# Optimization experiments

Measured on AMD Instinct MI355X. Metric: run time of the kernel, lower is better.

## Reference

```python
import jax, jax.numpy as jnp
import numpy as np

H = 1024          # rnn hidden dim
D = H // 2        # coarse/fine half
E = H // 8        # embed dim = 128
COND = H // 2     # conditioning (upsampled mel) dim = 512
EPS = 1e-5
TILE = 16


def _bn(x, scale, offset):
    # haiku BatchNorm, training mode: batch stats over (N, L)
    mean = jnp.mean(x, axis=(0, 1), keepdims=True)
    var = jnp.mean(jnp.square(x), axis=(0, 1), keepdims=True) - jnp.square(mean)
    return scale * (x - mean) * jax.lax.rsqrt(var + EPS) + offset


def _conv(x, w, rate=1):
    return jax.lax.conv_general_dilated(
        x, w, window_strides=(1,), padding='VALID', rhs_dilation=(rate,),
        dimension_numbers=('NWC', 'WIO', 'NWC'))


def _up(x, w, stride):
    # Conv1DTranspose with kernel 1, SAME padding: scatter x@w to positions i*stride
    N, L, _ = x.shape
    y = jnp.einsum('nlc,cd->nld', x, w)
    out = jnp.zeros((N, L, stride, y.shape[-1]), y.dtype).at[:, :, 0, :].set(y)
    return out.reshape(N, L * stride, y.shape[-1])


def _iw_mask():
    m = jnp.ones((COND + 3 * E, 3 * H), jnp.float32)
    for j in (0, 2, 4):  # coarse_t embed cannot see coarse half of u, r, e gates
        m = m.at[-E:, j * D:(j + 1) * D].set(0.0)
    return m


def _forward(x, mel, conv_in_w, bn0_s, bn0_o, dconv1_w, bn1_s, bn1_o,
             dconv2_w, bn2_s, bn2_o, up1_w, bn3_s, bn3_o, up2_w, bn4_s, bn4_o,
             up3_w, bn5_s, bn5_o, I_W, I_b, R_w, R_b,
             O1_w, O1_b, O2_w, O2_b, O3_w, O3_b, O4_w, O4_b, c_embed, f_embed):
    # ---- UpsampleNetwork ----
    h = jax.nn.relu(_bn(_conv(mel, conv_in_w), bn0_s, bn0_o))
    r1 = jax.nn.relu(_bn(_conv(h, dconv1_w, rate=2), bn1_s, bn1_o))
    h = h[:, 1:-1] + r1
    r2 = jax.nn.relu(_bn(_conv(h, dconv2_w, rate=4), bn2_s, bn2_o))
    h = h[:, 2:-2] + r2
    h = jax.nn.relu(_bn(_up(h, up1_w, 2), bn3_s, bn3_o))
    h = jax.nn.relu(_bn(_up(h, up2_w, 2), bn4_s, bn4_o))
    h = jax.nn.relu(_bn(_up(h, up3_w, 4), bn5_s, bn5_o))
    N, Lm, Dm = h.shape
    mel_up = jnp.tile(h[:, :, None, :], (1, 1, TILE, 1)).reshape(N, Lm * TILE, Dm)

    # ---- WaveRNNOriginal.__call__ (teacher-forced GRU) ----
    coarse, fine, coarse_t = x[..., 0], x[..., 1], x[..., 2]
    inputs = jnp.concatenate(
        (mel_up, c_embed[coarse], f_embed[fine], c_embed[coarse_t]), axis=-1)
    # precompute input projection for all timesteps  [N, L, 3H]
    ix = jnp.einsum('nli,ij->nlj', inputs, I_W * _iw_mask()) + I_b.reshape(1, 1, -1)
    ix_t = jnp.swapaxes(ix, 0, 1)  # time-major [L, N, 3H]
    h0 = jnp.zeros((N, H), ix.dtype)

    def step(hx, xt):
        u1, r1_, e1 = jnp.split(hx @ R_w + R_b, 3, axis=-1)
        u2, r2_, e2 = jnp.split(xt, 3, axis=-1)
        ut = jax.nn.sigmoid(u1 + u2)
        rt = jax.nn.sigmoid(r1_ + r2_)
        et = jnp.tanh(rt * e1 + e2)
        ht = ut * hx + (1.0 - ut) * et
        return ht, ht

    _, hs = jax.lax.scan(step, h0, ix_t)
    hs = jnp.swapaxes(hs, 0, 1)              # [N, L, H]
    yc, yf = jnp.split(hs, 2, axis=-1)       # [N, L, H/2] each
    clog = jax.nn.relu(yc @ O1_w + O1_b) @ O2_w + O2_b
    flog = jax.nn.relu(yf @ O3_w + O3_b) @ O4_w + O4_b
    logits = jnp.stack((clog, flog), axis=-1)  # [N, L, 256, 2]
    return jax.nn.log_softmax(logits, axis=-2)


def setup_inputs():
    key = jax.random.key(0)
    ks = jax.random.split(key, 24)
    n = jax.random.normal
    N, T = 2, 24
    L = (T - 8) * 256  # 4096
    inp = {
        'x': jax.random.randint(ks[0], (N, L, 3), 0, 256),
        'mel': n(ks[1], (N, T, 80), jnp.float32),
        'conv_in_w': n(ks[2], (3, 80, 512)) * 0.05,
        'dconv1_w': n(ks[3], (2, 512, 512)) * 0.05,
        'dconv2_w': n(ks[4], (2, 512, 512)) * 0.05,
        'up1_w': n(ks[5], (512, 512)) * 0.05,
        'up2_w': n(ks[6], (512, 512)) * 0.05,
        'up3_w': n(ks[7], (512, COND)) * 0.05,
        'I_W': n(ks[8], (COND + 3 * E, 3 * H)) * 0.03,
        'I_b': jnp.zeros((3 * H,)),
        'R_w': n(ks[9], (H, 3 * H)) * 0.03,
        'R_b': jnp.zeros((3 * H,)),
        'O1_w': n(ks[10], (D, D)) * 0.05,
        'O1_b': jnp.zeros((D,)),
        'O2_w': n(ks[11], (D, 256)) * 0.05,
        'O2_b': jnp.zeros((256,)),
        'O3_w': n(ks[12], (D, D)) * 0.05,
        'O3_b': jnp.zeros((D,)),
        'O4_w': n(ks[13], (D, 256)) * 0.05,
        'O4_b': jnp.zeros((256,)),
        'c_embed': n(ks[14], (256, E)) * 0.1,
        'f_embed': n(ks[15], (256, E)) * 0.1,
    }
    for i in range(6):
        c = COND if i == 5 else 512
        inp[f'bn{i}_s'] = jnp.ones((c,))
        inp[f'bn{i}_o'] = jnp.zeros((c,))
    return inp


def reference(x, mel, conv_in_w, dconv1_w, dconv2_w, up1_w, up2_w, up3_w,
              I_W, I_b, R_w, R_b, O1_w, O1_b, O2_w, O2_b, O3_w, O3_b,
              O4_w, O4_b, c_embed, f_embed,
              bn0_s, bn0_o, bn1_s, bn1_o, bn2_s, bn2_o,
              bn3_s, bn3_o, bn4_s, bn4_o, bn5_s, bn5_o):
    return _forward(x, mel, conv_in_w, bn0_s, bn0_o, dconv1_w, bn1_s, bn1_o,
                    dconv2_w, bn2_s, bn2_o, up1_w, bn3_s, bn3_o, up2_w, bn4_s,
                    bn4_o, up3_w, bn5_s, bn5_o, I_W, I_b, R_w, R_b,
                    O1_w, O1_b, O2_w, O2_b, O3_w, O3_b, O4_w, O4_b,
                    c_embed, f_embed)
```

## Files before the change

### kernel.cpp

```cpp
#include <hip/hip_runtime.h>
#include <hip/hip_bf16.h>
#include <math.h>

__device__ __forceinline__ float bf2f(unsigned short u) {
  unsigned int x = ((unsigned int)u) << 16;
  return __builtin_bit_cast(float, x);
}
__device__ __forceinline__ unsigned short f2bf(float f) {
  unsigned int x = __builtin_bit_cast(unsigned int, f);
  unsigned int lsb = (x >> 16) & 1u;
  x += 0x7fffu + lsb;
  return (unsigned short)(x >> 16);
}
template <bool BF>
__device__ __forceinline__ float ld(const void* p, size_t i) {
  if (BF) return bf2f(((const unsigned short*)p)[i]);
  return ((const float*)p)[i];
}

#define SCOPE_AGENT __HIP_MEMORY_SCOPE_AGENT
typedef unsigned long long ull;

__global__ void k_init(const unsigned int* bn0s, ull* sbuf, int* dt) {
  int t = threadIdx.x;
  for (int i = t; i < 4096; i += 256) sbuf[i] = 0ULL;
  if (t == 0) dt[0] = (bn0s[0] == 0x3F803F80u) ? 1 : 0;
}
__global__ void k_zero(uint4* hq4) {
  hq4[(size_t)blockIdx.x * 256 + threadIdx.x] = make_uint4(0u, 0u, 0u, 0u);
}

template <bool BF>
__device__ void conv_in_body(const void* mel, const void* w, float* out) {
  int idx = blockIdx.x * 256 + threadIdx.x;
  if (idx >= 2 * 22 * 512) return;
  int c = idx & 511, l = (idx >> 9) % 22, n = idx / (22 * 512);
  float acc = 0.f;
  for (int kw = 0; kw < 3; kw++) {
    size_t mrow = (size_t)(n * 24 + l + kw) * 80;
    size_t wrow = (size_t)kw * 80 * 512 + c;
#pragma unroll 4
    for (int i = 0; i < 80; i++)
      acc += ld<BF>(mel, mrow + i) * ld<BF>(w, wrow + (size_t)i * 512);
  }
  out[idx] = acc;
}
__global__ void k_conv_in(const void* mel, const void* w, float* out, const int* dt) {
  if (dt[0]) conv_in_body<true>(mel, w, out); else conv_in_body<false>(mel, w, out);
}

template <bool BF>
__device__ void dconv_body(const float* in, const void* w, float* out,
                           int Lin, int Lout, int rate) {
  int idx = blockIdx.x * 256 + threadIdx.x;
  if (idx >= 2 * Lout * 512) return;
  int c = idx & 511, l = (idx >> 9) % Lout, n = idx / (Lout * 512);
  float acc = 0.f;
  for (int kw = 0; kw < 2; kw++) {
    const float* irow = in + (n * Lin + l + kw * rate) * 512;
    size_t wrow = (size_t)kw * 512 * 512 + c;
#pragma unroll 4
    for (int i = 0; i < 512; i++)
      acc += irow[i] * ld<BF>(w, wrow + (size_t)i * 512);
  }
  out[idx] = acc;
}
__global__ void k_dconv(const float* in, const void* w, float* out,
                        int Lin, int Lout, int rate, const int* dt) {
  if (dt[0]) dconv_body<true>(in, w, out, Lin, Lout, rate);
  else dconv_body<false>(in, w, out, Lin, Lout, rate);
}

template <bool BF>
__device__ void up_body(const float* in, const void* w, float* out, int Lin, int stride) {
  int Lout = Lin * stride;
  int idx = blockIdx.x * 256 + threadIdx.x;
  if (idx >= 2 * Lout * 512) return;
  int c = idx & 511, lo = (idx >> 9) % Lout, n = idx / (Lout * 512);
  if (lo % stride) { out[idx] = 0.f; return; }
  const float* irow = in + (n * Lin + lo / stride) * 512;
  float acc = 0.f;
#pragma unroll 4
  for (int i = 0; i < 512; i++) acc += irow[i] * ld<BF>(w, (size_t)i * 512 + c);
  out[idx] = acc;
}
__global__ void k_up(const float* in, const void* w, float* out,
                     int Lin, int stride, const int* dt) {
  if (dt[0]) up_body<true>(in, w, out, Lin, stride);
  else up_body<false>(in, w, out, Lin, stride);
}

__global__ void k_bnstats(const float* __restrict__ x, float* __restrict__ st, int NL) {
  int c = blockIdx.x * 256 + threadIdx.x;
  if (c >= 512) return;
  float s = 0.f, s2 = 0.f;
  for (int r = 0; r < NL; r++) { float v = x[r * 512 + c]; s += v; s2 += v * v; }
  float m = s / (float)NL;
  float var = s2 / (float)NL - m * m;
  st[c] = m;
  st[512 + c] = rsqrtf(var + 1e-5f);
}

template <bool BF>
__device__ void bnrelu_body(const float* x, float* y, const float* st,
                            const void* sc, const void* of,
                            const float* res, int resL, int shift, int L) {
  int idx = blockIdx.x * 256 + threadIdx.x;
  if (idx >= 2 * L * 512) return;
  int c = idx & 511, l = (idx >> 9) % L, n = idx / (L * 512);
  float v = (x[idx] - st[c]) * st[512 + c] * ld<BF>(sc, c) + ld<BF>(of, c);
  v = fmaxf(v, 0.f);
  if (res) v += res[(n * resL + l + shift) * 512 + c];
  y[idx] = v;
}
__global__ void k_bnrelu(const float* x, float* y, const float* st,
                         const void* sc, const void* of,
                         const float* res, int resL, int shift, int L, const int* dt) {
  if (dt[0]) bnrelu_body<true>(x, y, st, sc, of, res, resL, shift, L);
  else bnrelu_body<false>(x, y, st, sc, of, res, resL, shift, L);
}

template <bool BF>
__device__ void M_body(const float* h5, const void* IW, const void* Ib,
                       const void* Rb, float* M, float* hl) {
  int bid = blockIdx.x;
  int rt = bid / 12, ct = bid % 12;
  int r0 = rt * 8, j = ct * 256 + threadIdx.x;
  const float4* src = (const float4*)(h5 + (size_t)r0 * 512);
  float4* dst = (float4*)hl;
  for (int q = threadIdx.x; q < 1024; q += 256) dst[q] = src[q];
  __syncthreads();
  float acc[8];
#pragma unroll
  for (int r = 0; r < 8; r++) acc[r] = 0.f;
  for (int k = 0; k < 512; k += 4) {
    float w0 = ld<BF>(IW, (size_t)k * 3072 + j);
    float w1 = ld<BF>(IW, (size_t)(k + 1) * 3072 + j);
    float w2 = ld<BF>(IW, (size_t)(k + 2) * 3072 + j);
    float w3 = ld<BF>(IW, (size_t)(k + 3) * 3072 + j);
#pragma unroll
    for (int r = 0; r < 8; r++) {
      float4 h4 = *(const float4*)(hl + r * 512 + k);
      acc[r] += h4.x * w0 + h4.y * w1 + h4.z * w2 + h4.w * w3;
    }
  }
  float bias = ld<BF>(Ib, j) + ((j < 2048) ? ld<BF>(Rb, j) : 0.f);
#pragma unroll
  for (int r = 0; r < 8; r++) M[(size_t)(r0 + r) * 3072 + j] = acc[r] + bias;
}
__global__ __launch_bounds__(256) void k_M(const float* h5, const void* IW,
                                           const void* Ib, const void* Rb,
                                           float* M, const int* dt) {
  __shared__ float hl[8 * 512];
  if (dt[0]) M_body<true>(h5, IW, Ib, Rb, M, hl);
  else M_body<false>(h5, IW, Ib, Rb, M, hl);
}

template <bool BF>
__device__ void T_body(const void* emb, const void* IW, int row0, int maskcoarse,
                       float* T, float* el) {
  int bid = blockIdx.x;
  int vt = bid / 12, ct = bid % 12;
  int v0 = vt * 8, j = ct * 256 + threadIdx.x;
  for (int q = threadIdx.x; q < 1024; q += 256)
    el[q] = ld<BF>(emb, (size_t)v0 * 128 + q);
  __syncthreads();
  float acc[8];
#pragma unroll
  for (int r = 0; r < 8; r++) acc[r] = 0.f;
  for (int k = 0; k < 128; k += 4) {
    float w0 = ld<BF>(IW, (size_t)(row0 + k) * 3072 + j);
    float w1 = ld<BF>(IW, (size_t)(row0 + k + 1) * 3072 + j);
    float w2 = ld<BF>(IW, (size_t)(row0 + k + 2) * 3072 + j);
    float w3 = ld<BF>(IW, (size_t)(row0 + k + 3) * 3072 + j);
#pragma unroll
    for (int r = 0; r < 8; r++) {
      float4 e4 = *(const float4*)(el + r * 128 + k);
      acc[r] += e4.x * w0 + e4.y * w1 + e4.z * w2 + e4.w * w3;
    }
  }
  bool mask = maskcoarse && ((j & 1023) < 512);
#pragma unroll
  for (int r = 0; r < 8; r++)
    T[(size_t)(v0 + r) * 3072 + j] = mask ? 0.f : acc[r];
}
__global__ __launch_bounds__(256) void k_T(const void* emb, const void* IW, int row0,
                                           int maskcoarse, float* T, const int* dt) {
  __shared__ float el[8 * 128];
  if (dt[0]) T_body<true>(emb, IW, row0, maskcoarse, T, el);
  else T_body<false>(emb, IW, row0, maskcoarse, T, el);
}

#define NWG 128
#define NEPI 128
template <bool BF>
__device__ void gru_body(const float* __restrict__ M, const float* __restrict__ T1,
                         const float* __restrict__ T2, const float* __restrict__ T3,
                         const int* __restrict__ x, const void* Rw, const void* Rb,
                         ull* sbuf, unsigned int* __restrict__ hq, float* hlds) {
  const int g = blockIdx.x, tid = threadIdx.x;
  const int n = g >> 6;
  const int il = tid >> 5, ks = tid & 31;
  const int i = (g & 63) * 16 + il;
  const int koff = ks * 32;
  const int k0 = tid * 2;
  const int lidx = (k0 >> 6) * 68 + (k0 & 63);

  float wreg[96];
#pragma unroll
  for (int gt = 0; gt < 3; gt++)
#pragma unroll
    for (int kk = 0; kk < 32; kk++)
      wreg[gt * 32 + kk] = ld<BF>(Rw, (size_t)(koff + kk) * 3072 + gt * 1024 + i);
  const float rbe = ld<BF>(Rb, 2048 + i);

  float hprev = 0.f;

  for (int t = 0; t < 4096; t++) {
    float* hb = hlds + (t & 1) * (16 * 68);

    float au = 0.f, ar = 0.f, ae = 0.f;
    if (ks == 0) {
      const int* xr = x + (n * 4096 + t) * 3;
      int ci = xr[0], fi = xr[1], cti = xr[2];
      const float* mr = M + (size_t)(n * 256 + (t >> 4)) * 3072;
      const float* p1 = T1 + (size_t)ci * 3072;
      const float* p2 = T2 + (size_t)fi * 3072;
      const float* p3 = T3 + (size_t)cti * 3072;
      au = mr[i] + p1[i] + p2[i] + p3[i];
      ar = mr[1024 + i] + p1[1024 + i] + p2[1024 + i] + p3[1024 + i];
      ae = mr[2048 + i] + p1[2048 + i] + p2[2048 + i] + p3[2048 + i];
    }

    const ull thr = (ull)(unsigned int)t << 32;
    ull* sb = sbuf + (size_t)(((t & 1) << 1) + n) * 1024 + k0;
    ull s0, s1;
    while (true) {
      s0 = __hip_atomic_load(sb + 0, __ATOMIC_RELAXED, SCOPE_AGENT);
      s1 = __hip_atomic_load(sb + 1, __ATOMIC_RELAXED, SCOPE_AGENT);
      if (s0 >= thr && s1 >= thr) break;
    }
    float2 h2;
    h2.x = __builtin_bit_cast(float, (unsigned int)s0);
    h2.y = __builtin_bit_cast(float, (unsigned int)s1);
    *(float2*)(hb + lidx) = h2;
    __syncthreads();

    float du = 0.f, dr = 0.f, de = 0.f;
    const float* hp = hb + (ks >> 1) * 68 + (ks & 1) * 32;
#pragma unroll
    for (int kk = 0; kk < 32; kk += 4) {
      float4 h4 = *(const float4*)(hp + kk);
      du += wreg[kk] * h4.x + wreg[kk + 1] * h4.y + wreg[kk + 2] * h4.z + wreg[kk + 3] * h4.w;
      dr += wreg[32 + kk] * h4.x + wreg[33 + kk] * h4.y + wreg[34 + kk] * h4.z + wreg[35 + kk] * h4.w;
      de += wreg[64 + kk] * h4.x + wreg[65 + kk] * h4.y + wreg[66 + kk] * h4.z + wreg[67 + kk] * h4.w;
    }
#pragma unroll
    for (int off = 16; off > 0; off >>= 1) {
      du += __shfl_xor(du, off, 32);
      dr += __shfl_xor(dr, off, 32);
      de += __shfl_xor(de, off, 32);
    }

    if (ks == 0) {
      float u = 1.f / (1.f + __expf(-(du + au)));
      float r = 1.f / (1.f + __expf(-(dr + ar)));
      float w = r * (de + rbe) + ae;
      float e = 1.f - 2.f / (__expf(2.f * w) + 1.f);
      float ht = u * hprev + (1.f - u) * e;
      hprev = ht;
      ull slot = ((ull)(unsigned int)(t + 1) << 32) |
                 (ull)__builtin_bit_cast(unsigned int, ht);
      __hip_atomic_store(
          sbuf + (size_t)((((t + 1) & 1) << 1) + n) * 1024 + i, slot,
          __ATOMIC_RELAXED, SCOPE_AGENT);
      unsigned int hv = ((unsigned int)f2bf(ht) << 16) | (unsigned int)(t + 1);
      __hip_atomic_store(hq + (size_t)(n * 4096 + t) * 1024 + i, hv,
                         __ATOMIC_RELAXED, SCOPE_AGENT);
    }
  }
}

template <bool BF>
__device__ void epi_body(const unsigned int* __restrict__ hq,
                         const void* O1w, const void* O1b,
                         const void* O3w, const void* O3b,
                         const void* O2w, const void* O2b,
                         const void* O4w, const void* O4b,
                         void* out, float* smem) {
  const int e = blockIdx.x - NWG, tid = threadIdx.x;
  float* hrow = smem;
  float* tmid = smem + 1024;
  float* red = smem + 2048;
  const int col = tid & 255;
  const bool isf = tid >= 256;
  const int base = isf ? 4 : 0;
  const void* W2 = isf ? O4w : O2w;
  const float b2 = isf ? ld<BF>(O4b, col) : ld<BF>(O2b, col);

  for (int tc = 0; tc < 32; tc++) {
    int t = tc * NEPI + e;
    for (int n = 0; n < 2; n++) {
      size_t row = (size_t)n * 4096 + t;
      const unsigned int* hp = hq + row * 1024 + tid * 2;
      unsigned int a, b;
      while (true) {
        a = __hip_atomic_load(hp + 0, __ATOMIC_RELAXED, SCOPE_AGENT);
        b = __hip_atomic_load(hp + 1, __ATOMIC_RELAXED, SCOPE_AGENT);
        if ((a & 0xffffu) && (b & 0xffffu)) break;
        __builtin_amdgcn_s_sleep(16);
      }
      float2 h2;
      h2.x = __builtin_bit_cast(float, a & 0xffff0000u);
      h2.y = __builtin_bit_cast(float, b & 0xffff0000u);
      *(float2*)(hrow + tid * 2) = h2;
      __syncthreads();

      float a1 = 0.f, a3 = 0.f;
#pragma unroll 4
      for (int k = 0; k < 512; k++) {
        a1 += hrow[k] * ld<BF>(O1w, (size_t)k * 512 + tid);
        a3 += hrow[512 + k] * ld<BF>(O3w, (size_t)k * 512 + tid);
      }
      tmid[tid] = fmaxf(a1 + ld<BF>(O1b, tid), 0.f);
      tmid[512 + tid] = fmaxf(a3 + ld<BF>(O3b, tid), 0.f);
      __syncthreads();

      float acc = 0.f;
      const float* tm = tmid + (isf ? 512 : 0);
#pragma unroll 4
      for (int j = 0; j < 512; j++)
        acc += tm[j] * ld<BF>(W2, (size_t)j * 256 + col);
      acc += b2;

      float v = acc;
#pragma unroll
      for (int off = 32; off > 0; off >>= 1) v = fmaxf(v, __shfl_xor(v, off));
      if ((tid & 63) == 0) red[tid >> 6] = v;
      __syncthreads();
      float m = fmaxf(fmaxf(red[base], red[base + 1]),
                      fmaxf(red[base + 2], red[base + 3]));
      __syncthreads();
      float s = __expf(acc - m);
#pragma unroll
      for (int off = 32; off > 0; off >>= 1) s += __shfl_xor(s, off);
      if ((tid & 63) == 0) red[tid >> 6] = s;
      __syncthreads();
      float ssum = red[base] + red[base + 1] + red[base + 2] + red[base + 3];
      float o = acc - m - logf(ssum);
      __syncthreads();
      if (BF) ((unsigned short*)out)[(row * 256 + col) * 2 + (isf ? 1 : 0)] = f2bf(o);
      else ((float*)out)[(row * 256 + col) * 2 + (isf ? 1 : 0)] = o;
    }
  }
}

__global__ __launch_bounds__(512, 1) void k_gru(
    const float* M, const float* T1, const float* T2, const float* T3,
    const int* x, const void* Rw, const void* Rb,
    ull* sbuf, unsigned int* hq,
    const void* O1w, const void* O1b, const void* O3w, const void* O3b,
    const void* O2w, const void* O2b, const void* O4w, const void* O4b,
    void* out, const int* dt) {
  __shared__ __align__(16) float smem[2176];
  if (dt[0]) {
    if (blockIdx.x < NWG) gru_body<true>(M, T1, T2, T3, x, Rw, Rb, sbuf, hq, smem);
    else epi_body<true>(hq, O1w, O1b, O3w, O3b, O2w, O2b, O4w, O4b, out, smem);
  } else {
    if (blockIdx.x < NWG) gru_body<false>(M, T1, T2, T3, x, Rw, Rb, sbuf, hq, smem);
    else epi_body<false>(hq, O1w, O1b, O3w, O3b, O2w, O2b, O4w, O4b, out, smem);
  }
}

extern "C" void kernel_launch(void* const* d_in, const int* in_sizes, int n_in,
                              void* d_out, int out_size, void* d_ws, size_t ws_size,
                              hipStream_t stream) {
  const int* x = (const int*)d_in[0];
  const void* mel = d_in[1];
  const void* conv_in_w = d_in[2];
  const void* dconv1_w = d_in[3];
  const void* dconv2_w = d_in[4];
  const void* up1_w = d_in[5];
  const void* up2_w = d_in[6];
  const void* up3_w = d_in[7];
  const void* IW = d_in[8];
  const void* Ib = d_in[9];
  const void* Rw = d_in[10];
  const void* Rb = d_in[11];
  const void* O1w = d_in[12];
  const void* O1b = d_in[13];
  const void* O2w = d_in[14];
  const void* O2b = d_in[15];
  const void* O3w = d_in[16];
  const void* O3b = d_in[17];
  const void* O4w = d_in[18];
  const void* O4b = d_in[19];
  const void* c_embed = d_in[20];
  const void* f_embed = d_in[21];
  const void* bns[6], *bno[6];
  for (int s = 0; s < 6; s++) {
    bns[s] = d_in[22 + 2 * s];
    bno[s] = d_in[23 + 2 * s];
  }

  float* ws = (float*)d_ws;
  float* A = ws;
  float* B = A + 262144;
  float* st = B + 262144;
  float* M = st + 1024;
  float* T1 = M + 1572864;
  float* T2 = T1 + 786432;
  float* T3 = T2 + 786432;
  ull* sbuf = (ull*)(T3 + 786432);
  int* dt = (int*)(sbuf + 4096);
  unsigned int* hq = (unsigned int*)(dt + 4);

  k_init<<<1, 256, 0, stream>>>((const unsigned int*)bns[0], sbuf, dt);
  k_zero<<<8192, 256, 0, stream>>>((uint4*)hq);

  k_conv_in<<<88, 256, 0, stream>>>(mel, conv_in_w, A, dt);
  k_bnstats<<<2, 256, 0, stream>>>(A, st, 44);
  k_bnrelu<<<88, 256, 0, stream>>>(A, A, st, bns[0], bno[0], nullptr, 0, 0, 22, dt);

  k_dconv<<<80, 256, 0, stream>>>(A, dconv1_w, B, 22, 20, 2, dt);
  k_bnstats<<<2, 256, 0, stream>>>(B, st, 40);
  k_bnrelu<<<80, 256, 0, stream>>>(B, B, st, bns[1], bno[1], A, 22, 1, 20, dt);

  k_dconv<<<64, 256, 0, stream>>>(B, dconv2_w, A, 20, 16, 4, dt);
  k_bnstats<<<2, 256, 0, stream>>>(A, st, 32);
  k_bnrelu<<<64, 256, 0, stream>>>(A, A, st, bns[2], bno[2], B, 20, 2, 16, dt);

  k_up<<<128, 256, 0, stream>>>(A, up1_w, B, 16, 2, dt);
  k_bnstats<<<2, 256, 0, stream>>>(B, st, 64);
  k_bnrelu<<<128, 256, 0, stream>>>(B, B, st, bns[3], bno[3], nullptr, 0, 0, 32, dt);

  k_up<<<256, 256, 0, stream>>>(B, up2_w, A, 32, 2, dt);
  k_bnstats<<<2, 256, 0, stream>>>(A, st, 128);
  k_bnrelu<<<256, 256, 0, stream>>>(A, A, st, bns[4], bno[4], nullptr, 0, 0, 64, dt);

  k_up<<<1024, 256, 0, stream>>>(A, up3_w, B, 64, 4, dt);
  k_bnstats<<<2, 256, 0, stream>>>(B, st, 512);
  k_bnrelu<<<1024, 256, 0, stream>>>(B, B, st, bns[5], bno[5], nullptr, 0, 0, 256, dt);

  k_M<<<768, 256, 0, stream>>>(B, IW, Ib, Rb, M, dt);
  k_T<<<384, 256, 0, stream>>>(c_embed, IW, 512, 0, T1, dt);
  k_T<<<384, 256, 0, stream>>>(f_embed, IW, 640, 0, T2, dt);
  k_T<<<384, 256, 0, stream>>>(c_embed, IW, 768, 1, T3, dt);

  k_gru<<<NWG + NEPI, 512, 0, stream>>>(M, T1, T2, T3, x, Rw, Rb, sbuf, hq,
                                        O1w, O1b, O3w, O3b, O2w, O2b, O4w, O4b,
                                        d_out, dt);

  (void)in_sizes; (void)n_in; (void)out_size; (void)ws_size;
}
```

Before: 9.622 ms.

## Replace per-element tagged hidden-state flags with per-block progress counters

GRU workgroups now store their hidden state as plain bf16 and publish a release-ordered progress counter every 64 timesteps. Epilogue blocks wait for all 64 producers of their batch with one wave and an acquire fence, where before every thread spun on tagged 32-bit words. This removes the large zeroing kernel and halves the hidden-state traffic. It also cuts the epilogue blocks from 128 to 64, and the GRU blocks gain an extra block-wide barrier every 64 steps, which can delay the epilogue start and add stalls to the critical recurrent path.

```diff
diff --git a/kernel.cpp b/kernel.cpp
--- a/kernel.cpp
+++ b/kernel.cpp
@@ -5,6 +5,12 @@
 __device__ __forceinline__ float bf2f(unsigned short u) {
   unsigned int x = ((unsigned int)u) << 16;
   return __builtin_bit_cast(float, x);
+}
+__device__ __forceinline__ float lo16(unsigned int u) {
+  return __builtin_bit_cast(float, u << 16);
+}
+__device__ __forceinline__ float hi16(unsigned int u) {
+  return __builtin_bit_cast(float, u & 0xffff0000u);
 }
 __device__ __forceinline__ unsigned short f2bf(float f) {
   unsigned int x = __builtin_bit_cast(unsigned int, f);
@@ -21,13 +27,11 @@
 #define SCOPE_AGENT __HIP_MEMORY_SCOPE_AGENT
 typedef unsigned long long ull;
 
-__global__ void k_init(const unsigned int* bn0s, ull* sbuf, int* dt) {
+__global__ void k_init(const unsigned int* bn0s, ull* sbuf, int* progress, int* dt) {
   int t = threadIdx.x;
   for (int i = t; i < 4096; i += 256) sbuf[i] = 0ULL;
+  for (int i = t; i < 2048; i += 256) progress[i] = 0;
   if (t == 0) dt[0] = (bn0s[0] == 0x3F803F80u) ? 1 : 0;
-}
-__global__ void k_zero(uint4* hq4) {
-  hq4[(size_t)blockIdx.x * 256 + threadIdx.x] = make_uint4(0u, 0u, 0u, 0u);
 }
 
 template <bool BF>
@@ -192,12 +196,13 @@
 }
 
 #define NWG 128
-#define NEPI 128
+#define NEPI 64
 template <bool BF>
 __device__ void gru_body(const float* __restrict__ M, const float* __restrict__ T1,
                          const float* __restrict__ T2, const float* __restrict__ T3,
                          const int* __restrict__ x, const void* Rw, const void* Rb,
-                         ull* sbuf, unsigned int* __restrict__ hq, float* hlds) {
+                         ull* sbuf, unsigned short* __restrict__ hs,
+                         int* progress, float* hlds) {
   const int g = blockIdx.x, tid = threadIdx.x;
   const int n = g >> 6;
   const int il = tid >> 5, ks = tid & 31;
@@ -274,15 +279,20 @@
       __hip_atomic_store(
           sbuf + (size_t)((((t + 1) & 1) << 1) + n) * 1024 + i, slot,
           __ATOMIC_RELAXED, SCOPE_AGENT);
-      unsigned int hv = ((unsigned int)f2bf(ht) << 16) | (unsigned int)(t + 1);
-      __hip_atomic_store(hq + (size_t)(n * 4096 + t) * 1024 + i, hv,
-                         __ATOMIC_RELAXED, SCOPE_AGENT);
-    }
-  }
-}
-
-template <bool BF>
-__device__ void epi_body(const unsigned int* __restrict__ hq,
+      hs[(size_t)(n * 4096 + t) * 1024 + i] = f2bf(ht);
+    }
+
+    if ((t & 63) == 63) {
+      __syncthreads();
+      if (tid == 0)
+        __hip_atomic_store(&progress[g * 16], t + 1, __ATOMIC_RELEASE, SCOPE_AGENT);
+    }
+  }
+}
+
+template <bool BF>
+__device__ void epi_body(const unsigned short* __restrict__ hs,
+                         const int* __restrict__ progress,
                          const void* O1w, const void* O1b,
                          const void* O3w, const void* O3b,
                          const void* O2w, const void* O2b,
@@ -292,28 +302,31 @@
   float* hrow = smem;
   float* tmid = smem + 1024;
   float* red = smem + 2048;
+  const int wave = tid >> 6, lane = tid & 63;
   const int col = tid & 255;
   const bool isf = tid >= 256;
   const int base = isf ? 4 : 0;
   const void* W2 = isf ? O4w : O2w;
   const float b2 = isf ? ld<BF>(O4b, col) : ld<BF>(O2b, col);
 
-  for (int tc = 0; tc < 32; tc++) {
-    int t = tc * NEPI + e;
+  for (int w = 0; w < 64; w++) {
+    int t = w * NEPI + e;
     for (int n = 0; n < 2; n++) {
       size_t row = (size_t)n * 4096 + t;
-      const unsigned int* hp = hq + row * 1024 + tid * 2;
-      unsigned int a, b;
-      while (true) {
-        a = __hip_atomic_load(hp + 0, __ATOMIC_RELAXED, SCOPE_AGENT);
-        b = __hip_atomic_load(hp + 1, __ATOMIC_RELAXED, SCOPE_AGENT);
-        if ((a & 0xffffu) && (b & 0xffffu)) break;
-        __builtin_amdgcn_s_sleep(16);
+      if (wave == 0) {
+        while (true) {
+          int p = __hip_atomic_load(&progress[(n * 64 + lane) * 16],
+                                    __ATOMIC_RELAXED, SCOPE_AGENT);
+          if (__all(p >= t + 1)) break;
+          __builtin_amdgcn_s_sleep(32);
+        }
+        __builtin_amdgcn_fence(__ATOMIC_ACQUIRE, "agent");
       }
-      float2 h2;
-      h2.x = __builtin_bit_cast(float, a & 0xffff0000u);
-      h2.y = __builtin_bit_cast(float, b & 0xffff0000u);
-      *(float2*)(hrow + tid * 2) = h2;
+      __syncthreads();
+
+      unsigned int pr = ((const unsigned int*)(hs + row * 1024))[tid];
+      hrow[tid * 2] = lo16(pr);
+      hrow[tid * 2 + 1] = hi16(pr);
       __syncthreads();
 
       float a1 = 0.f, a3 = 0.f;
@@ -336,7 +349,7 @@
       float v = acc;
 #pragma unroll
       for (int off = 32; off > 0; off >>= 1) v = fmaxf(v, __shfl_xor(v, off));
-      if ((tid & 63) == 0) red[tid >> 6] = v;
+      if (lane == 0) red[wave] = v;
       __syncthreads();
       float m = fmaxf(fmaxf(red[base], red[base + 1]),
                       fmaxf(red[base + 2], red[base + 3]));
@@ -344,7 +357,7 @@
       float s = __expf(acc - m);
 #pragma unroll
       for (int off = 32; off > 0; off >>= 1) s += __shfl_xor(s, off);
-      if ((tid & 63) == 0) red[tid >> 6] = s;
+      if (lane == 0) red[wave] = s;
       __syncthreads();
       float ssum = red[base] + red[base + 1] + red[base + 2] + red[base + 3];
       float o = acc - m - logf(ssum);
@@ -358,17 +371,21 @@
 __global__ __launch_bounds__(512, 1) void k_gru(
     const float* M, const float* T1, const float* T2, const float* T3,
     const int* x, const void* Rw, const void* Rb,
-    ull* sbuf, unsigned int* hq,
+    ull* sbuf, unsigned short* hs, int* progress,
     const void* O1w, const void* O1b, const void* O3w, const void* O3b,
     const void* O2w, const void* O2b, const void* O4w, const void* O4b,
     void* out, const int* dt) {
   __shared__ __align__(16) float smem[2176];
   if (dt[0]) {
-    if (blockIdx.x < NWG) gru_body<true>(M, T1, T2, T3, x, Rw, Rb, sbuf, hq, smem);
-    else epi_body<true>(hq, O1w, O1b, O3w, O3b, O2w, O2b, O4w, O4b, out, smem);
+    if (blockIdx.x < NWG)
+      gru_body<true>(M, T1, T2, T3, x, Rw, Rb, sbuf, hs, progress, smem);
+    else
+      epi_body<true>(hs, progress, O1w, O1b, O3w, O3b, O2w, O2b, O4w, O4b, out, smem);
   } else {
-    if (blockIdx.x < NWG) gru_body<false>(M, T1, T2, T3, x, Rw, Rb, sbuf, hq, smem);
-    else epi_body<false>(hq, O1w, O1b, O3w, O3b, O2w, O2b, O4w, O4b, out, smem);
+    if (blockIdx.x < NWG)
+      gru_body<false>(M, T1, T2, T3, x, Rw, Rb, sbuf, hs, progress, smem);
+    else
+      epi_body<false>(hs, progress, O1w, O1b, O3w, O3b, O2w, O2b, O4w, O4b, out, smem);
   }
 }
 
@@ -412,11 +429,11 @@
   float* T2 = T1 + 786432;
   float* T3 = T2 + 786432;
   ull* sbuf = (ull*)(T3 + 786432);
-  int* dt = (int*)(sbuf + 4096);
-  unsigned int* hq = (unsigned int*)(dt + 4);
-
-  k_init<<<1, 256, 0, stream>>>((const unsigned int*)bns[0], sbuf, dt);
-  k_zero<<<8192, 256, 0, stream>>>((uint4*)hq);
+  int* progress = (int*)(sbuf + 4096);
+  int* dt = progress + 2048;
+  unsigned short* hs = (unsigned short*)(dt + 4);
+
+  k_init<<<1, 256, 0, stream>>>((const unsigned int*)bns[0], sbuf, progress, dt);
 
   k_conv_in<<<88, 256, 0, stream>>>(mel, conv_in_w, A, dt);
   k_bnstats<<<2, 256, 0, stream>>>(A, st, 44);
@@ -447,7 +464,7 @@
   k_T<<<384, 256, 0, stream>>>(f_embed, IW, 640, 0, T2, dt);
   k_T<<<384, 256, 0, stream>>>(c_embed, IW, 768, 1, T3, dt);
 
-  k_gru<<<NWG + NEPI, 512, 0, stream>>>(M, T1, T2, T3, x, Rw, Rb, sbuf, hq,
+  k_gru<<<NWG + NEPI, 512, 0, stream>>>(M, T1, T2, T3, x, Rw, Rb, sbuf, hs, progress,
                                         O1w, O1b, O3w, O3b, O2w, O2b, O4w, O4b,
                                         d_out, dt);
 
```

Result: no change. 9.627 ms (+0.1%).
